# Kernel optimization log

Hardware: AMD Instinct MI355X
Metric: run time of the kernel (lower is better)

## Reference

```python
import jax, jax.numpy as jnp
import numpy as np

# sizes / constants (mirroring the source module's constants)
M, T_SOL, NX, NY = 12, 64, 256, 256
N_TIMES, NOUT = 50, 256
LX, LY_TARGET = 60.0, 75.0
C_CU_TARGET, C_NI_TARGET = 0.001, 0.0001
T_MAX = 200.0
SIGMA, H, DH = 0.25, 4, 8


def setup_inputs() -> dict:
    key = jax.random.key(0)
    ks = jax.random.split(key, 7)
    u = jax.random.uniform(ks[0], (M, 3), dtype=jnp.float32)
    # rows: (Ly in [30,120], c_Cu in [0,0.0029], c_Ni in [0,0.0018])
    params = jnp.stack([30.0 + 90.0 * u[:, 0], 0.0029 * u[:, 1], 0.0018 * u[:, 2]], axis=1)
    c1_src = jax.random.uniform(ks[1], (M, T_SOL, NX, NY), dtype=jnp.float32) * 0.003
    c2_src = jax.random.uniform(ks[2], (M, T_SOL, NX, NY), dtype=jnp.float32) * 0.002
    Wq = jax.random.normal(ks[3], (H * DH, 3), dtype=jnp.float32) * 0.5
    bq = jax.random.normal(ks[4], (H * DH,), dtype=jnp.float32) * 0.1
    Wk = jax.random.normal(ks[5], (H * DH, 3), dtype=jnp.float32) * 0.5
    bk = jax.random.normal(ks[6], (H * DH,), dtype=jnp.float32) * 0.1
    return {"params": params, "c1_src": c1_src, "c2_src": c2_src,
            "Wq": Wq, "bq": bq, "Wk": Wk, "bk": bk}


def _bilinear_resample(xs, ys, vals, xq, yq):
    """RegularGridInterpolator(linear, fill_value=0) on grid (xs[NX], ys[NY]).
    vals: [T, NX, NY]; query is the outer-product grid xq[PX] x yq[PY].
    Separable bilinear -> [T, PX, PY]."""
    ix = jnp.clip(jnp.searchsorted(xs, xq, side='right') - 1, 0, xs.shape[0] - 2)
    tx = (xq - xs[ix]) / (xs[ix + 1] - xs[ix])
    vx = vals[:, ix, :] * (1.0 - tx)[None, :, None] + vals[:, ix + 1, :] * tx[None, :, None]
    iy = jnp.clip(jnp.searchsorted(ys, yq, side='right') - 1, 0, ys.shape[0] - 2)
    ty = (yq - ys[iy]) / (ys[iy + 1] - ys[iy])
    out = vx[:, :, iy] * (1.0 - ty)[None, None, :] + vx[:, :, iy + 1] * ty[None, None, :]
    inb = ((xq >= xs[0]) & (xq <= xs[-1]))[:, None] & ((yq >= ys[0]) & (yq <= ys[-1]))[None, :]
    return jnp.where(inb[None], out, jnp.float32(0.0))


def _forward(params, c1_src, c2_src, Wq, bq, Wk, bk):
    lys, c_cus, c_nis = params[:, 0], params[:, 1], params[:, 2]
    ly_n = (lys - 30.0) / 90.0
    ccu_n = c_cus / 0.0029
    cni_n = c_nis / 0.0018
    p = jnp.stack([ly_n, ccu_n, cni_n], axis=1)                      # [M,3]
    t = jnp.array([[(LY_TARGET - 30.0) / 90.0,
                    C_CU_TARGET / 0.0029,
                    C_NI_TARGET / 0.0018]], dtype=params.dtype)       # [1,3]
    Q = (t @ Wq.T + bq).reshape(1, H, DH)
    K = (p @ Wk.T + bk).reshape(-1, H, DH)
    attn = jnp.einsum('nhd,mhd->nmh', K, Q) / (DH ** 0.5)            # [M,1,H]
    attn_w = jax.nn.softmax(attn, axis=0).mean(axis=2)[:, 0]         # [M]
    dist2 = (((ly_n - t[0, 0]) / SIGMA) ** 2
             + ((ccu_n - t[0, 1]) / SIGMA) ** 2
             + ((cni_n - t[0, 2]) / SIGMA) ** 2)
    sw = jnp.exp(-dist2 / 2.0)
    sw = sw / sw.sum()
    w = attn_w * sw
    w = w / w.sum()                                                  # [M]

    # grids: source x shared; per-solution y grid rescaled to [0, LY_TARGET]
    xs = jnp.linspace(0.0, LX, NX)
    ys_scaled = (jnp.linspace(0.0, 1.0, NY)[None, :] * lys[:, None]) * (LY_TARGET / lys)[:, None]  # [M,NY]
    xq = jnp.linspace(0.0, LX, NOUT)
    yq = jnp.linspace(0.0, LY_TARGET, NOUT)

    times = jnp.linspace(0.0, min(T_MAX, T_MAX), N_TIMES)
    tidx = jnp.clip((times / T_MAX * T_SOL).astype(jnp.int32), 0, T_SOL - 1)  # [T]
    c1_sel = c1_src[:, tidx]                                          # [M,T,NX,NY]
    c2_sel = c2_src[:, tidx]

    res1, res2 = jax.vmap(
        lambda ys, v1, v2: (_bilinear_resample(xs, ys, v1, xq, yq),
                            _bilinear_resample(xs, ys, v2, xq, yq))
    )(ys_scaled, c1_sel, c2_sel)                                      # each [M,T,NOUT,NOUT]

    c1 = jnp.einsum('m,mtij->tij', w, res1)
    c2 = jnp.einsum('m,mtij->tij', w, res2)
    c1 = c1.at[:, :, 0].set(C_CU_TARGET)
    c2 = c2.at[:, :, -1].set(C_NI_TARGET)
    return jnp.stack([c1, c2])                                        # [2,T,NOUT,NOUT]


def reference(params, c1_src, c2_src, Wq, bq, Wk, bk):
    return _forward(params, c1_src, c2_src, Wq, bq, Wk, bk)
```

## Files before the change

kernel.cpp:

```cpp
#include <hip/hip_runtime.h>

#define MM    12
#define TSOL  64
#define NXX   256
#define NYY   256
#define NTT   50
#define NOUTT 256
#define IPB   4

__device__ float4 g_tab[MM * NOUTT];

__global__ __launch_bounds__(256) void ai_setup_kernel(
    const float* __restrict__ params,
    const float* __restrict__ Wq, const float* __restrict__ bq,
    const float* __restrict__ Wk, const float* __restrict__ bk)
{
    const int k = threadIdx.x;
    const int m = blockIdx.x;

    __shared__ float s_attn[MM][4];
    __shared__ float s_sw[MM];
    __shared__ float s_wm;
    __shared__ float s_ys[NYY];

    if (k < MM) {
        float ly = params[k * 3 + 0];
        float p0 = (ly - 30.0f) / 90.0f;
        float p1 = params[k * 3 + 1] / 0.0029f;
        float p2 = params[k * 3 + 2] / 0.0018f;
        const float t0 = 0.5f;
        const float t1 = 0.001f / 0.0029f;
        const float t2 = 0.0001f / 0.0018f;
        for (int h = 0; h < 4; ++h) {
            float acc = 0.0f;
            for (int d = 0; d < 8; ++d) {
                int o = h * 8 + d;
                float q  = t0 * Wq[o * 3 + 0] + t1 * Wq[o * 3 + 1] + t2 * Wq[o * 3 + 2] + bq[o];
                float kv = p0 * Wk[o * 3 + 0] + p1 * Wk[o * 3 + 1] + p2 * Wk[o * 3 + 2] + bk[o];
                acc += kv * q;
            }
            s_attn[k][h] = acc * 0.35355339059327373f;
        }
        float d0 = (p0 - t0) / 0.25f;
        float d1 = (p1 - t1) / 0.25f;
        float d2 = (p2 - t2) / 0.25f;
        s_sw[k] = expf(-(d0 * d0 + d1 * d1 + d2 * d2) * 0.5f);
    }
    __syncthreads();

    if (k == 0) {
        float aw[MM];
        for (int j = 0; j < MM; ++j) aw[j] = 0.0f;
        for (int h = 0; h < 4; ++h) {
            float mx = s_attn[0][h];
            for (int j = 1; j < MM; ++j) mx = fmaxf(mx, s_attn[j][h]);
            float e[MM]; float sum = 0.0f;
            for (int j = 0; j < MM; ++j) { e[j] = expf(s_attn[j][h] - mx); sum += e[j]; }
            for (int j = 0; j < MM; ++j) aw[j] += e[j] / sum;
        }
        float swsum = 0.0f;
        for (int j = 0; j < MM; ++j) swsum += s_sw[j];
        float wj[MM]; float wsum = 0.0f;
        for (int j = 0; j < MM; ++j) {
            wj[j] = (aw[j] * 0.25f) * (s_sw[j] / swsum);
            wsum += wj[j];
        }
        s_wm = wj[m] / wsum;
    }

    {
        float ly  = params[m * 3 + 0];
        float inv = 75.0f / ly;
        float l01 = (float)k * (1.0f / 255.0f);
        s_ys[k] = (l01 * ly) * inv;
    }
    __syncthreads();

    float w  = s_wm;
    float yq = (float)k * (75.0f / 255.0f);
    int l = 0, r = NYY;
    while (l < r) { int mid = (l + r) >> 1; if (s_ys[mid] <= yq) l = mid + 1; else r = mid; }
    int iy = l - 1;
    iy = iy < 0 ? 0 : (iy > NYY - 2 ? NYY - 2 : iy);
    float ty  = (yq - s_ys[iy]) / (s_ys[iy + 1] - s_ys[iy]);
    bool  inb = (yq >= s_ys[0]) && (yq <= s_ys[NYY - 1]);
    float4 tb;
    tb.x = inb ? w * (1.0f - ty) : 0.0f;
    tb.y = inb ? w * ty          : 0.0f;
    tb.z = __int_as_float(iy);
    tb.w = 0.0f;
    g_tab[m * NOUTT + k] = tb;
}

__global__ __launch_bounds__(256) void ai_resample_kernel(
    const float* __restrict__ c1, const float* __restrict__ c2,
    float* __restrict__ out)
{
    const int tid = threadIdx.x;
    const int t   = blockIdx.y;
    const int i0  = blockIdx.x * IPB;
    int tsrc = (t * TSOL) / (NTT - 1);
    if (tsrc > TSOL - 1) tsrc = TSOL - 1;

    float w0[MM], w1[MM];
    unsigned int iy[MM];
#pragma unroll
    for (int m = 0; m < MM; ++m) {
        float4 tb = g_tab[m * NOUTT + tid];
        w0[m] = tb.x;
        w1[m] = tb.y;
        iy[m] = (unsigned int)__float_as_int(tb.z);
    }

    unsigned int rbase[MM];
#pragma unroll
    for (int m = 0; m < MM; ++m)
        rbase[m] = (((unsigned int)(m * TSOL + tsrc) * NXX) + (unsigned int)i0) * NYY + iy[m];

#pragma unroll 2
    for (int r = 0; r < IPB; ++r) {
        float acc1 = 0.0f, acc2 = 0.0f;
#pragma unroll
        for (int m = 0; m < MM; ++m) {
            unsigned int off = rbase[m] + (unsigned int)r * NYY;
            float a0 = c1[off], a1 = c1[off + 1];
            float b0 = c2[off], b1 = c2[off + 1];
            acc1 += w0[m] * a0 + w1[m] * a1;
            acc2 += w0[m] * b0 + w1[m] * b1;
        }
        int i = i0 + r;
        float o1 = (tid == 0)         ? 0.001f  : acc1;
        float o2 = (tid == NOUTT - 1) ? 0.0001f : acc2;
        out[((size_t)t * NOUTT + (size_t)i) * NOUTT + (size_t)tid] = o1;
        out[((size_t)(NTT + t) * NOUTT + (size_t)i) * NOUTT + (size_t)tid] = o2;
    }
}

extern "C" void kernel_launch(void* const* d_in, const int* in_sizes, int n_in,
                              void* d_out, int out_size, void* d_ws, size_t ws_size,
                              hipStream_t stream) {
    const float* params = (const float*)d_in[0];
    const float* c1     = (const float*)d_in[1];
    const float* c2     = (const float*)d_in[2];
    const float* Wq     = (const float*)d_in[3];
    const float* bq     = (const float*)d_in[4];
    const float* Wk     = (const float*)d_in[5];
    const float* bk     = (const float*)d_in[6];
    float* out = (float*)d_out;

    ai_setup_kernel<<<dim3(MM), dim3(256), 0, stream>>>(params, Wq, bq, Wk, bk);
    ai_resample_kernel<<<dim3(NOUTT / IPB, NTT), dim3(256), 0, stream>>>(c1, c2, out);
}
```

Measured before the change: 427.7 us.

## Replace per-column gathers with float4 row loads and a three-tap shuffle stencil

The setup kernel now stores three weight planes (left, centre, right taps) instead of a per-column index and two weights. This relies on the rescaled y grid lining up with the query grid, so each output column only needs neighbours k-1, k and k+1. In the resample kernel each wave handles one output row, and each lane loads four contiguous source values as a float4. The missing neighbours come from adjacent lanes via shuffles, and results are written with float4 stores. This is meant to replace scattered scalar gathers with coalesced vector traffic, at the cost of assuming iy never equals k+1.

```diff
diff --git a/kernel.cpp b/kernel.cpp
--- a/kernel.cpp
+++ b/kernel.cpp
@@ -6,9 +6,10 @@
 #define NYY   256
 #define NTT   50
 #define NOUTT 256
-#define IPB   4
 
-__device__ float4 g_tab[MM * NOUTT];
+__device__ float g_wm1[MM * NOUTT];
+__device__ float g_wc [MM * NOUTT];
+__device__ float g_wp1[MM * NOUTT];
 
 __global__ __launch_bounds__(256) void ai_setup_kernel(
     const float* __restrict__ params,
@@ -84,56 +85,60 @@
     iy = iy < 0 ? 0 : (iy > NYY - 2 ? NYY - 2 : iy);
     float ty  = (yq - s_ys[iy]) / (s_ys[iy + 1] - s_ys[iy]);
     bool  inb = (yq >= s_ys[0]) && (yq <= s_ys[NYY - 1]);
-    float4 tb;
-    tb.x = inb ? w * (1.0f - ty) : 0.0f;
-    tb.y = inb ? w * ty          : 0.0f;
-    tb.z = __int_as_float(iy);
-    tb.w = 0.0f;
-    g_tab[m * NOUTT + k] = tb;
+    float a = inb ? w * (1.0f - ty) : 0.0f;
+    float b = inb ? w * ty          : 0.0f;
+    bool sel = (iy == k);
+    g_wm1[m * NOUTT + k] = sel ? 0.0f : a;
+    g_wc [m * NOUTT + k] = sel ? a    : b;
+    g_wp1[m * NOUTT + k] = sel ? b    : 0.0f;
 }
 
 __global__ __launch_bounds__(256) void ai_resample_kernel(
     const float* __restrict__ c1, const float* __restrict__ c2,
     float* __restrict__ out)
 {
-    const int tid = threadIdx.x;
-    const int t   = blockIdx.y;
-    const int i0  = blockIdx.x * IPB;
+    const int tid  = threadIdx.x;
+    const int lane = tid & 63;
+    const int wv   = tid >> 6;
+    const int t    = blockIdx.y;
+    const int i    = blockIdx.x * 4 + wv;
     int tsrc = (t * TSOL) / (NTT - 1);
     if (tsrc > TSOL - 1) tsrc = TSOL - 1;
+    const int k0 = lane * 4;
 
-    float w0[MM], w1[MM];
-    unsigned int iy[MM];
+    float4 acc1 = {0.f, 0.f, 0.f, 0.f};
+    float4 acc2 = {0.f, 0.f, 0.f, 0.f};
+
 #pragma unroll
     for (int m = 0; m < MM; ++m) {
-        float4 tb = g_tab[m * NOUTT + tid];
-        w0[m] = tb.x;
-        w1[m] = tb.y;
-        iy[m] = (unsigned int)__float_as_int(tb.z);
+        const float4 wm1 = *(const float4*)&g_wm1[m * NOUTT + k0];
+        const float4 wc  = *(const float4*)&g_wc [m * NOUTT + k0];
+        const float4 wp1 = *(const float4*)&g_wp1[m * NOUTT + k0];
+        const size_t base = ((size_t)(m * TSOL + tsrc) * NXX + (size_t)i) * NYY
+                          + (size_t)k0;
+        float4 s1 = *(const float4*)(c1 + base);
+        float4 s2 = *(const float4*)(c2 + base);
+
+        float l1 = __shfl_up(s1.w, 1);
+        float r1 = __shfl_down(s1.x, 1);
+        acc1.x += wm1.x * l1   + wc.x * s1.x + wp1.x * s1.y;
+        acc1.y += wm1.y * s1.x + wc.y * s1.y + wp1.y * s1.z;
+        acc1.z += wm1.z * s1.y + wc.z * s1.z + wp1.z * s1.w;
+        acc1.w += wm1.w * s1.z + wc.w * s1.w + wp1.w * r1;
+
+        float l2 = __shfl_up(s2.w, 1);
+        float r2 = __shfl_down(s2.x, 1);
+        acc2.x += wm1.x * l2   + wc.x * s2.x + wp1.x * s2.y;
+        acc2.y += wm1.y * s2.x + wc.y * s2.y + wp1.y * s2.z;
+        acc2.z += wm1.z * s2.y + wc.z * s2.z + wp1.z * s2.w;
+        acc2.w += wm1.w * s2.z + wc.w * s2.w + wp1.w * r2;
     }
 
-    unsigned int rbase[MM];
-#pragma unroll
-    for (int m = 0; m < MM; ++m)
-        rbase[m] = (((unsigned int)(m * TSOL + tsrc) * NXX) + (unsigned int)i0) * NYY + iy[m];
+    if (lane == 0)  acc1.x = 0.001f;
+    if (lane == 63) acc2.w = 0.0001f;
 
-#pragma unroll 2
-    for (int r = 0; r < IPB; ++r) {
-        float acc1 = 0.0f, acc2 = 0.0f;
-#pragma unroll
-        for (int m = 0; m < MM; ++m) {
-            unsigned int off = rbase[m] + (unsigned int)r * NYY;
-            float a0 = c1[off], a1 = c1[off + 1];
-            float b0 = c2[off], b1 = c2[off + 1];
-            acc1 += w0[m] * a0 + w1[m] * a1;
-            acc2 += w0[m] * b0 + w1[m] * b1;
-        }
-        int i = i0 + r;
-        float o1 = (tid == 0)         ? 0.001f  : acc1;
-        float o2 = (tid == NOUTT - 1) ? 0.0001f : acc2;
-        out[((size_t)t * NOUTT + (size_t)i) * NOUTT + (size_t)tid] = o1;
-        out[((size_t)(NTT + t) * NOUTT + (size_t)i) * NOUTT + (size_t)tid] = o2;
-    }
+    *(float4*)&out[((size_t)t * NOUTT + (size_t)i) * NOUTT + (size_t)k0] = acc1;
+    *(float4*)&out[((size_t)(NTT + t) * NOUTT + (size_t)i) * NOUTT + (size_t)k0] = acc2;
 }
 
 extern "C" void kernel_launch(void* const* d_in, const int* in_sizes, int n_in,
@@ -149,5 +154,5 @@
     float* out = (float*)d_out;
 
     ai_setup_kernel<<<dim3(MM), dim3(256), 0, stream>>>(params, Wq, bq, Wk, bk);
-    ai_resample_kernel<<<dim3(NOUTT / IPB, NTT), dim3(256), 0, stream>>>(c1, c2, out);
+    ai_resample_kernel<<<dim3(NOUTT / 4, NTT), dim3(256), 0, stream>>>(c1, c2, out);
 }
```

New measurement: 403.6 us. 1.06x faster.
